# Kernel tuning notes

Hardware: AMD Instinct MI355X
Metric: run time of the kernel (lower is better)

## Reference

```python
import jax, jax.numpy as jnp
import numpy as np

N_NODES = 100000
N_EDGES = 1600000
IN_RAW = 64
HID = 128


def setup_inputs() -> dict:
    key = jax.random.key(0)
    ks = jax.random.split(key, 16)
    inp = {
        "x": jax.random.normal(ks[0], (N_NODES, IN_RAW), dtype=jnp.float32),
        "edge_index": jax.random.randint(ks[1], (2, N_EDGES), 0, N_NODES, dtype=jnp.int64),
        "user_ids": jax.random.randint(ks[2], (N_NODES,), 0, 10000, dtype=jnp.int64),
        "locations": jax.random.randint(ks[3], (N_NODES,), 0, 1000, dtype=jnp.int64),
        "time_features": jax.random.normal(ks[4], (N_NODES, 4), dtype=jnp.float32),
        # embeddings / encoders
        "user_emb_table": jax.random.normal(ks[5], (10000, 32), dtype=jnp.float32) * 0.02,
        "loc_emb_table": jax.random.normal(ks[6], (1000, 16), dtype=jnp.float32) * 0.02,
        "W_time": jax.random.normal(ks[7], (4, 16), dtype=jnp.float32) * 0.1,
        "b_time": jnp.zeros((16,), dtype=jnp.float32),
        # SAGEConv 1: lin_l (aggregated, with bias), lin_r (root, no bias)
        "W1_l": jax.random.normal(ks[8], (HID, HID), dtype=jnp.float32) * (1.0 / np.sqrt(HID)),
        "b1": jnp.zeros((HID,), dtype=jnp.float32),
        "W1_r": jax.random.normal(ks[9], (HID, HID), dtype=jnp.float32) * (1.0 / np.sqrt(HID)),
        # SAGEConv 2
        "W2_l": jax.random.normal(ks[10], (HID, HID), dtype=jnp.float32) * (1.0 / np.sqrt(HID)),
        "b2": jnp.zeros((HID,), dtype=jnp.float32),
        "W2_r": jax.random.normal(ks[11], (HID, HID), dtype=jnp.float32) * (1.0 / np.sqrt(HID)),
        # classifier
        "Wc": jax.random.normal(ks[12], (HID, 1), dtype=jnp.float32) * (1.0 / np.sqrt(HID)),
        "bc": jnp.zeros((1,), dtype=jnp.float32),
    }
    return inp


def _sage_conv(h, src, dst, W_l, b_l, W_r, n_nodes):
    # mean aggregation of source features onto targets (PyG SAGEConv default)
    msg_sum = jax.ops.segment_sum(h[src], dst, num_segments=n_nodes)  # [N, D]
    deg = jax.ops.segment_sum(jnp.ones((src.shape[0],), h.dtype), dst, num_segments=n_nodes)
    agg = msg_sum / jnp.maximum(deg, 1.0)[:, None]
    return agg @ W_l + b_l + h @ W_r


def reference(x, edge_index, user_ids, locations, time_features,
              user_emb_table, loc_emb_table, W_time, b_time,
              W1_l, b1, W1_r, W2_l, b2, W2_r, Wc, bc):
    n = x.shape[0]
    src, dst = edge_index[0], edge_index[1]
    user_emb = user_emb_table[user_ids]            # [N, 32]
    loc_emb = loc_emb_table[locations]             # [N, 16]
    time_emb = time_features @ W_time + b_time     # [N, 16]
    h = jnp.concatenate([x, user_emb, loc_emb, time_emb], axis=-1)  # [N, 128]
    h = jax.nn.relu(_sage_conv(h, src, dst, W1_l, b1, W1_r, n))  # dropout = identity (eval)
    h = jax.nn.relu(_sage_conv(h, src, dst, W2_l, b2, W2_r, n))
    return jax.nn.sigmoid(h @ Wc + bc)  # [N, 1]
```

## Files before the change

### kernel.cpp

```cpp
#include <hip/hip_runtime.h>
#include <math.h>

#define N_NODES 100000
#define HID 128
#define NB 782
#define CAP 4096
#define NBLK 256
#define BTILE 6250
#define SUBCAP 32
#define SCAP 3072
#define WPB 64

typedef __attribute__((ext_vector_type(8))) short bf16x8;
typedef __attribute__((ext_vector_type(4))) float f32x4;
typedef __attribute__((ext_vector_type(2))) float f32x2;

__device__ __forceinline__ unsigned short f2bf(float f) {
  union { float f; unsigned u; } v; v.f = f;
  unsigned r = v.u + 0x7FFFu + ((v.u >> 16) & 1u);
  return (unsigned short)(r >> 16);
}
__device__ __forceinline__ unsigned packbf(float lo, float hi) {
  return (unsigned)f2bf(lo) | ((unsigned)f2bf(hi) << 16);
}
__device__ __forceinline__ unsigned pkfp8x4(float a, float b, float c, float d) {
  int v = __builtin_amdgcn_cvt_pk_fp8_f32(a, b, 0, false);
  v = __builtin_amdgcn_cvt_pk_fp8_f32(c, d, v, true);
  return (unsigned)v;
}
__device__ __forceinline__ float bflo(unsigned u) {
  union { unsigned u; float f; } v; v.u = u << 16; return v.f;
}
__device__ __forceinline__ float bfhi(unsigned u) {
  union { unsigned u; float f; } v; v.u = u & 0xFFFF0000u; return v.f;
}
__device__ __forceinline__ void acc_add_fp8(float* a, unsigned w) {
  f32x2 p0 = __builtin_amdgcn_cvt_pk_f32_fp8((int)w, false);
  f32x2 p1 = __builtin_amdgcn_cvt_pk_f32_fp8((int)w, true);
  a[0] += p0.x; a[1] += p0.y; a[2] += p1.x; a[3] += p1.y;
}
__device__ __forceinline__ void acc_add_row(float* a, uint4 u) {
  acc_add_fp8(a + 0, u.x);
  acc_add_fp8(a + 4, u.y);
  acc_add_fp8(a + 8, u.z);
  acc_add_fp8(a + 12, u.w);
}

__global__ __launch_bounds__(256) void k_embed(
    const float* __restrict__ x, const int* __restrict__ uid,
    const int* __restrict__ lid, const float* __restrict__ timef,
    const float* __restrict__ utab, const float* __restrict__ ltab,
    const float* __restrict__ Wt, const float* __restrict__ bt,
    unsigned short* __restrict__ h0, unsigned char* __restrict__ h0f8) {
  int t = threadIdx.x;
  int v = blockIdx.x * 16 + (t >> 4);
  int g = t & 15;
  if (v >= N_NODES) return;
  float val[8];
  if (g < 8) {
    const float4* xp = (const float4*)&x[(size_t)v * 64 + g * 8];
    float4 a = xp[0], b = xp[1];
    val[0] = a.x; val[1] = a.y; val[2] = a.z; val[3] = a.w;
    val[4] = b.x; val[5] = b.y; val[6] = b.z; val[7] = b.w;
  } else if (g < 12) {
    const float4* up = (const float4*)&utab[(size_t)uid[v] * 32 + (g - 8) * 8];
    float4 a = up[0], b = up[1];
    val[0] = a.x; val[1] = a.y; val[2] = a.z; val[3] = a.w;
    val[4] = b.x; val[5] = b.y; val[6] = b.z; val[7] = b.w;
  } else if (g < 14) {
    const float4* lp = (const float4*)&ltab[(size_t)lid[v] * 16 + (g - 12) * 8];
    float4 a = lp[0], b = lp[1];
    val[0] = a.x; val[1] = a.y; val[2] = a.z; val[3] = a.w;
    val[4] = b.x; val[5] = b.y; val[6] = b.z; val[7] = b.w;
  } else {
    int c0 = (g - 14) * 8;
    float4 tf = *(const float4*)&timef[(size_t)v * 4];
#pragma unroll
    for (int i = 0; i < 8; ++i) {
      int c = c0 + i;
      val[i] = bt[c] + tf.x * Wt[c] + tf.y * Wt[16 + c] + tf.z * Wt[32 + c] +
               tf.w * Wt[48 + c];
    }
  }
  uint4 ob;
  ob.x = packbf(val[0], val[1]);
  ob.y = packbf(val[2], val[3]);
  ob.z = packbf(val[4], val[5]);
  ob.w = packbf(val[6], val[7]);
  *(uint4*)&h0[(size_t)v * 128 + g * 8] = ob;
  uint2 of;
  of.x = pkfp8x4(val[0], val[1], val[2], val[3]);
  of.y = pkfp8x4(val[4], val[5], val[6], val[7]);
  *(uint2*)&h0f8[(size_t)v * 128 + g * 8] = of;
}

__global__ __launch_bounds__(512) void k_bucket(
    const int* __restrict__ src, const int* __restrict__ dst,
    int* __restrict__ gcnt, unsigned* __restrict__ bdata2, int E) {
  __shared__ int hcnt[NB];
  int t = threadIdx.x;
  int blk = blockIdx.x;
  int e0 = blk * BTILE;
  int e1 = min(e0 + BTILE, E);
  for (int i = t; i < NB; i += 512) hcnt[i] = 0;
  __syncthreads();
#pragma unroll 4
  for (int e = e0 + t; e < e1; e += 512) {
    int d = dst[e], s = src[e];
    int b = d >> 7;
    int pos = atomicAdd(&hcnt[b], 1);
    if (pos < SUBCAP)
      bdata2[((size_t)blk * NB + b) * SUBCAP + pos] =
          ((unsigned)s << 7) | (unsigned)(d & 127);
  }
  __syncthreads();
  for (int i = t; i < NB; i += 512)
    gcnt[blk * NB + i] = hcnt[i];
}

__global__ __launch_bounds__(256) void k_bfill(
    const int* __restrict__ gcnt, const unsigned* __restrict__ bdata2,
    int* __restrict__ rstart, int* __restrict__ rdeg, int* __restrict__ col,
    const float* __restrict__ W1l, const float* __restrict__ W1r,
    const float* __restrict__ W2l, const float* __restrict__ W2r,
    unsigned short* __restrict__ WT) {
  int b = blockIdx.x;
  int t = threadIdx.x;
  if (b >= NB) {
    int lin = ((b - NB) * 256 + t) * 4;
    int m = lin >> 14;
    int rem = lin & 16383;
    int f = rem >> 7;
    int k0 = rem & 127;
    const float* W = (m == 0) ? W1l : (m == 1) ? W1r : (m == 2) ? W2l : W2r;
    unsigned short o[4];
#pragma unroll
    for (int j = 0; j < 4; ++j) o[j] = f2bf(W[(size_t)(k0 + j) * 128 + f]);
    uint2 pk;
    pk.x = (unsigned)o[0] | ((unsigned)o[1] << 16);
    pk.y = (unsigned)o[2] | ((unsigned)o[3] << 16);
    *(uint2*)&WT[m * 16384 + f * 128 + k0] = pk;
    return;
  }
  __shared__ unsigned sdata[SCAP];
  __shared__ int soff[NBLK];
  __shared__ int scnt[NBLK];
  __shared__ int wsum[4];
  __shared__ int lcnt[128];
  __shared__ int wtot;
  int lane = t & 63, wv = t >> 6;

  int c = (t < NBLK) ? min(gcnt[t * NB + b], SUBCAP) : 0;
  int x = c;
#pragma unroll
  for (int off = 1; off < 64; off <<= 1) {
    int v = __shfl_up(x, off);
    if (lane >= off) x += v;
  }
  if (lane == 63) wsum[wv] = x;
  __syncthreads();
  int add = 0;
#pragma unroll
  for (int k = 0; k < 4; ++k)
    if (k < wv) add += wsum[k];
  x += add;
  int tot = min(wsum[0] + wsum[1] + wsum[2] + wsum[3], SCAP);
  if (t < NBLK) { soff[t] = x - c; scnt[t] = c; }
  if (t < 128) lcnt[t] = 0;
  __syncthreads();

  for (int i = t; i < NBLK * 8; i += 256) {
    int j = i >> 3, p4 = (i & 7) * 4;
    int cj = scnt[j];
    if (p4 < cj) {
      uint4 v = *(const uint4*)&bdata2[((size_t)j * NB + b) * SUBCAP + p4];
      int bs = soff[j] + p4;
      int n = min(4, cj - p4);
      unsigned vv[4] = {v.x, v.y, v.z, v.w};
#pragma unroll
      for (int e = 0; e < 4; ++e)
        if (e < n && bs + e < SCAP) sdata[bs + e] = vv[e];
    }
  }
  __syncthreads();

  for (int i = t; i < tot; i += 256) atomicAdd(&lcnt[sdata[i] & 127u], 1);
  __syncthreads();

  int node0 = b * 128;
  int base = b * CAP;
  if (t < 128) {
    int cc = lcnt[t];
    int xx = cc;
#pragma unroll
    for (int off = 1; off < 64; off <<= 1) {
      int v = __shfl_up(xx, off);
      if (lane >= off) xx += v;
    }
    if (t == 63) wtot = xx;
    __syncthreads();
    if (t >= 64) xx += wtot;
    int excl = xx - cc;
    if (node0 + t < N_NODES) {
      rstart[node0 + t] = base + excl;
      rdeg[node0 + t] = cc;
    }
    lcnt[t] = excl;
  } else {
    __syncthreads();
  }
  __syncthreads();
  for (int i = t; i < tot; i += 256) {
    unsigned v = sdata[i];
    int pos = base + atomicAdd(&lcnt[v & 127u], 1);
    col[pos] = (int)(v >> 7);
  }
}

__global__ __launch_bounds__(256) void k_agg(
    const unsigned char* __restrict__ hf8, const int* __restrict__ rstart,
    const int* __restrict__ rdeg, const int* __restrict__ col,
    unsigned short* __restrict__ agg) {
  int t = threadIdx.x;
  int v = blockIdx.x * 32 + (t >> 3);
  int q = t & 7;
  if (v >= N_NODES) return;
  int s0 = rstart[v];
  int deg = rdeg[v];
  int s1 = s0 + deg;
  const uint4* h8 = (const uint4*)hf8;
  float acc[16];
#pragma unroll
  for (int i = 0; i < 16; ++i) acc[i] = 0.f;
  int j = s0;
  for (; j + 4 <= s1; j += 4) {
    uint4 r0 = h8[(size_t)col[j] * 8 + q];
    uint4 r1 = h8[(size_t)col[j + 1] * 8 + q];
    uint4 r2 = h8[(size_t)col[j + 2] * 8 + q];
    uint4 r3 = h8[(size_t)col[j + 3] * 8 + q];
    acc_add_row(acc, r0);
    acc_add_row(acc, r1);
    acc_add_row(acc, r2);
    acc_add_row(acc, r3);
  }
  for (; j < s1; ++j) acc_add_row(acc, h8[(size_t)col[j] * 8 + q]);
  float inv = 1.f / (float)(deg > 0 ? deg : 1);
  uint4 o0, o1;
  o0.x = packbf(acc[0] * inv, acc[1] * inv);
  o0.y = packbf(acc[2] * inv, acc[3] * inv);
  o0.z = packbf(acc[4] * inv, acc[5] * inv);
  o0.w = packbf(acc[6] * inv, acc[7] * inv);
  o1.x = packbf(acc[8] * inv, acc[9] * inv);
  o1.y = packbf(acc[10] * inv, acc[11] * inv);
  o1.z = packbf(acc[12] * inv, acc[13] * inv);
  o1.w = packbf(acc[14] * inv, acc[15] * inv);
  ((uint4*)agg)[(size_t)v * 16 + q * 2] = o0;
  ((uint4*)agg)[(size_t)v * 16 + q * 2 + 1] = o1;
}

template <bool CLS>
__global__ __launch_bounds__(256, 4) void k_gemm(
    const unsigned short* __restrict__ agg, const unsigned short* __restrict__ hin,
    const unsigned short* __restrict__ WlT, const unsigned short* __restrict__ WrT,
    const float* __restrict__ bias, unsigned short* __restrict__ hout,
    unsigned char* __restrict__ houtf8,
    const float* __restrict__ Wc, const float* __restrict__ bc,
    float* __restrict__ out) {
  __shared__ unsigned short SB[2 * 64 * 136];
  unsigned short* As = SB;
  unsigned short* Hs = SB + 64 * 136;
  unsigned short* Ot = SB;
  float* zred = (float*)SB;
  int t = threadIdx.x;
  int lane = t & 63;
  int wave = t >> 6;
  int wn = wave * 32;
  int l15 = lane & 15;
  int quad = lane >> 4;
  int mbase = blockIdx.x * 64;

  {
    int r = t >> 2, seg = t & 3;
    int gn = mbase + r;
    uint4 av[4], hv[4];
    if (gn < N_NODES) {
      const uint4* ap = (const uint4*)(agg + (size_t)gn * 128 + seg * 32);
      const uint4* hp = (const uint4*)(hin + (size_t)gn * 128 + seg * 32);
#pragma unroll
      for (int i = 0; i < 4; ++i) { av[i] = ap[i]; hv[i] = hp[i]; }
    } else {
#pragma unroll
      for (int i = 0; i < 4; ++i) { av[i] = make_uint4(0,0,0,0); hv[i] = make_uint4(0,0,0,0); }
    }
#pragma unroll
    for (int i = 0; i < 4; ++i) {
      *(uint4*)&As[r * 136 + seg * 32 + i * 8] = av[i];
      *(uint4*)&Hs[r * 136 + seg * 32 + i * 8] = hv[i];
    }
  }
  __syncthreads();

  f32x4 acc4[4][2];
#pragma unroll
  for (int i = 0; i < 4; ++i)
#pragma unroll
    for (int j = 0; j < 2; ++j) acc4[i][j] = (f32x4){0.f, 0.f, 0.f, 0.f};

#pragma unroll
  for (int ks = 0; ks < 4; ++ks) {
    int kb = ks * 32 + quad * 8;
    bf16x8 bL[2], bR[2];
#pragma unroll
    for (int jn = 0; jn < 2; ++jn) {
      int f = wn + jn * 16 + l15;
      bL[jn] = *(const bf16x8*)&WlT[(size_t)f * 128 + kb];
      bR[jn] = *(const bf16x8*)&WrT[(size_t)f * 128 + kb];
    }
    bf16x8 aA[4], aH[4];
#pragma unroll
    for (int im = 0; im < 4; ++im) {
      aA[im] = *(const bf16x8*)&As[(im * 16 + l15) * 136 + kb];
      aH[im] = *(const bf16x8*)&Hs[(im * 16 + l15) * 136 + kb];
    }
#pragma unroll
    for (int im = 0; im < 4; ++im)
#pragma unroll
      for (int jn = 0; jn < 2; ++jn)
        acc4[im][jn] = __builtin_amdgcn_mfma_f32_16x16x32_bf16(
            aA[im], bL[jn], acc4[im][jn], 0, 0, 0);
#pragma unroll
    for (int im = 0; im < 4; ++im)
#pragma unroll
      for (int jn = 0; jn < 2; ++jn)
        acc4[im][jn] = __builtin_amdgcn_mfma_f32_16x16x32_bf16(
            aH[im], bR[jn], acc4[im][jn], 0, 0, 0);
  }

  float bv[2];
#pragma unroll
  for (int jn = 0; jn < 2; ++jn) bv[jn] = bias[wn + jn * 16 + l15];

  __syncthreads();

  if (!CLS) {
#pragma unroll
    for (int im = 0; im < 4; ++im)
#pragma unroll
      for (int rr = 0; rr < 4; ++rr) {
        int rloc = im * 16 + quad * 4 + rr;
#pragma unroll
        for (int jn = 0; jn < 2; ++jn)
          Ot[rloc * 136 + wn + jn * 16 + l15] =
              f2bf(fmaxf(acc4[im][jn][rr] + bv[jn], 0.f));
      }
    __syncthreads();
    int r = t >> 2, seg = t & 3;
    int node = mbase + r;
    if (node < N_NODES) {
      uint4 d0[4];
      const uint4* srcp = (const uint4*)&Ot[r * 136 + seg * 32];
      uint4* dstp = (uint4*)&hout[(size_t)node * 128 + seg * 32];
#pragma unroll
      for (int i = 0; i < 4; ++i) { d0[i] = srcp[i]; dstp[i] = d0[i]; }
      unsigned w[8];
#pragma unroll
      for (int i = 0; i < 4; ++i) {
        unsigned u[4] = {d0[i].x, d0[i].y, d0[i].z, d0[i].w};
#pragma unroll
        for (int p = 0; p < 2; ++p) {
          w[i * 2 + p] = pkfp8x4(bflo(u[p * 2]), bfhi(u[p * 2]),
                                 bflo(u[p * 2 + 1]), bfhi(u[p * 2 + 1]));
        }
      }
      uint4* fp = (uint4*)&houtf8[(size_t)node * 128 + seg * 32];
      fp[0] = make_uint4(w[0], w[1], w[2], w[3]);
      fp[1] = make_uint4(w[4], w[5], w[6], w[7]);
    }
  } else {
    float wcv[2];
#pragma unroll
    for (int jn = 0; jn < 2; ++jn) wcv[jn] = Wc[wn + jn * 16 + l15];
#pragma unroll
    for (int im = 0; im < 4; ++im) {
#pragma unroll
      for (int rr = 0; rr < 4; ++rr) {
        float p = 0.f;
#pragma unroll
        for (int jn = 0; jn < 2; ++jn)
          p += fmaxf(acc4[im][jn][rr] + bv[jn], 0.f) * wcv[jn];
        p += __shfl_xor(p, 1);
        p += __shfl_xor(p, 2);
        p += __shfl_xor(p, 4);
        p += __shfl_xor(p, 8);
        if (l15 == 0) zred[wave * 64 + im * 16 + quad * 4 + rr] = p;
      }
    }
    __syncthreads();
    if (t < 64) {
      int node = mbase + t;
      if (node < N_NODES) {
        float z = zred[t] + zred[64 + t] + zred[128 + t] + zred[192 + t] + bc[0];
        out[node] = 1.f / (1.f + expf(-z));
      }
    }
  }
}

extern "C" void kernel_launch(void* const* d_in, const int* in_sizes, int n_in,
                              void* d_out, int out_size, void* d_ws, size_t ws_size,
                              hipStream_t stream) {
  const float* x     = (const float*)d_in[0];
  const int*   eidx  = (const int*)d_in[1];
  const int*   uid   = (const int*)d_in[2];
  const int*   lid   = (const int*)d_in[3];
  const float* timef = (const float*)d_in[4];
  const float* utab  = (const float*)d_in[5];
  const float* ltab  = (const float*)d_in[6];
  const float* Wt    = (const float*)d_in[7];
  const float* bt    = (const float*)d_in[8];
  const float* W1l   = (const float*)d_in[9];
  const float* b1    = (const float*)d_in[10];
  const float* W1r   = (const float*)d_in[11];
  const float* W2l   = (const float*)d_in[12];
  const float* b2    = (const float*)d_in[13];
  const float* W2r   = (const float*)d_in[14];
  const float* Wc    = (const float*)d_in[15];
  const float* bc    = (const float*)d_in[16];
  float* out = (float*)d_out;

  const int E = in_sizes[1] / 2;
  const int* src = eidx;
  const int* dst = eidx + E;

  char* ws = (char*)d_ws;
  size_t off = 0;
  auto alloc = [&](size_t bytes) -> void* {
    void* p = ws + off;
    off += (bytes + 255) & ~(size_t)255;
    return p;
  };
  const size_t HBYTES = (size_t)N_NODES * 128 * sizeof(unsigned short);
  const size_t FBYTES = (size_t)N_NODES * 128;
  unsigned short* h0  = (unsigned short*)alloc(HBYTES);
  unsigned short* h1  = (unsigned short*)alloc(HBYTES);
  unsigned short* agg = (unsigned short*)alloc(HBYTES);
  unsigned char* h0f8 = (unsigned char*)alloc(FBYTES);
  unsigned char* h1f8 = (unsigned char*)alloc(FBYTES);
  unsigned short* WT  = (unsigned short*)alloc(4 * 16384 * sizeof(unsigned short));
  unsigned* bdata2    = (unsigned*)alloc((size_t)NBLK * NB * SUBCAP * 4);
  int* gcnt           = (int*)alloc((size_t)NBLK * NB * 4);
  int* col            = (int*)alloc((size_t)NB * CAP * 4);
  int* rstart         = (int*)alloc((size_t)N_NODES * 4);
  int* rdeg           = (int*)alloc((size_t)N_NODES * 4);
  (void)ws_size; (void)n_in; (void)out_size;

  k_bucket<<<NBLK, 512, 0, stream>>>(src, dst, gcnt, bdata2, E);
  k_embed<<<(N_NODES + 15) / 16, 256, 0, stream>>>(x, uid, lid, timef, utab, ltab, Wt, bt,
                                                   h0, h0f8);
  k_bfill<<<NB + WPB, 256, 0, stream>>>(gcnt, bdata2, rstart, rdeg, col,
                                        W1l, W1r, W2l, W2r, WT);

  k_agg<<<(N_NODES + 31) / 32, 256, 0, stream>>>(h0f8, rstart, rdeg, col, agg);
  k_gemm<false><<<(N_NODES + 63) / 64, 256, 0, stream>>>(
      agg, h0, WT, WT + 16384, b1, h1, h1f8, nullptr, nullptr, nullptr);

  k_agg<<<(N_NODES + 31) / 32, 256, 0, stream>>>(h1f8, rstart, rdeg, col, agg);
  k_gemm<true><<<(N_NODES + 63) / 64, 256, 0, stream>>>(
      agg, h1, WT + 32768, WT + 49152, b2, nullptr, nullptr, Wc, bc, out);
}
```

Before: 284.9 us.

## Fuse neighbor aggregation into the SAGE GEMM and merge bucketing with embedding

The mean-aggregation gather now runs inside the GEMM kernel and writes the bf16 aggregate straight into shared memory, which removes the global agg buffer and its write-then-read round trip plus two kernel launches. Edge bucketing and node embedding are merged into one launch with a block-index split, and the embed path moves from 256 to 512 threads per block. The tradeoff is that the GEMM kernel now carries the irregular gather latency with only 256 threads per 64-row tile, which may hurt latency hiding compared with the separate aggregation kernel.

```diff
diff --git a/kernel.cpp b/kernel.cpp
--- a/kernel.cpp
+++ b/kernel.cpp
@@ -10,6 +10,7 @@
 #define SUBCAP 32
 #define SCAP 3072
 #define WPB 64
+#define EBLK 3125
 
 typedef __attribute__((ext_vector_type(8))) short bf16x8;
 typedef __attribute__((ext_vector_type(4))) float f32x4;
@@ -46,14 +47,37 @@
   acc_add_fp8(a + 12, u.w);
 }
 
-__global__ __launch_bounds__(256) void k_embed(
+__global__ __launch_bounds__(512) void k_bktembed(
+    const int* __restrict__ src, const int* __restrict__ dst,
+    int* __restrict__ gcnt, unsigned* __restrict__ bdata2, int E,
     const float* __restrict__ x, const int* __restrict__ uid,
     const int* __restrict__ lid, const float* __restrict__ timef,
     const float* __restrict__ utab, const float* __restrict__ ltab,
     const float* __restrict__ Wt, const float* __restrict__ bt,
     unsigned short* __restrict__ h0, unsigned char* __restrict__ h0f8) {
+  __shared__ int hcnt[NB];
   int t = threadIdx.x;
-  int v = blockIdx.x * 16 + (t >> 4);
+  if (blockIdx.x < NBLK) {
+    int blk = blockIdx.x;
+    int e0 = blk * BTILE;
+    int e1 = min(e0 + BTILE, E);
+    for (int i = t; i < NB; i += 512) hcnt[i] = 0;
+    __syncthreads();
+#pragma unroll 4
+    for (int e = e0 + t; e < e1; e += 512) {
+      int d = dst[e], s = src[e];
+      int b = d >> 7;
+      int pos = atomicAdd(&hcnt[b], 1);
+      if (pos < SUBCAP)
+        bdata2[((size_t)blk * NB + b) * SUBCAP + pos] =
+            ((unsigned)s << 7) | (unsigned)(d & 127);
+    }
+    __syncthreads();
+    for (int i = t; i < NB; i += 512)
+      gcnt[blk * NB + i] = hcnt[i];
+    return;
+  }
+  int v = (blockIdx.x - NBLK) * 32 + (t >> 4);
   int g = t & 15;
   if (v >= N_NODES) return;
   float val[8];
@@ -94,30 +118,6 @@
   *(uint2*)&h0f8[(size_t)v * 128 + g * 8] = of;
 }
 
-__global__ __launch_bounds__(512) void k_bucket(
-    const int* __restrict__ src, const int* __restrict__ dst,
-    int* __restrict__ gcnt, unsigned* __restrict__ bdata2, int E) {
-  __shared__ int hcnt[NB];
-  int t = threadIdx.x;
-  int blk = blockIdx.x;
-  int e0 = blk * BTILE;
-  int e1 = min(e0 + BTILE, E);
-  for (int i = t; i < NB; i += 512) hcnt[i] = 0;
-  __syncthreads();
-#pragma unroll 4
-  for (int e = e0 + t; e < e1; e += 512) {
-    int d = dst[e], s = src[e];
-    int b = d >> 7;
-    int pos = atomicAdd(&hcnt[b], 1);
-    if (pos < SUBCAP)
-      bdata2[((size_t)blk * NB + b) * SUBCAP + pos] =
-          ((unsigned)s << 7) | (unsigned)(d & 127);
-  }
-  __syncthreads();
-  for (int i = t; i < NB; i += 512)
-    gcnt[blk * NB + i] = hcnt[i];
-}
-
 __global__ __launch_bounds__(256) void k_bfill(
     const int* __restrict__ gcnt, const unsigned* __restrict__ bdata2,
     int* __restrict__ rstart, int* __restrict__ rdeg, int* __restrict__ col,
@@ -217,50 +217,11 @@
   }
 }
 
-__global__ __launch_bounds__(256) void k_agg(
+template <bool CLS>
+__global__ __launch_bounds__(256, 4) void k_aggemm(
     const unsigned char* __restrict__ hf8, const int* __restrict__ rstart,
     const int* __restrict__ rdeg, const int* __restrict__ col,
-    unsigned short* __restrict__ agg) {
-  int t = threadIdx.x;
-  int v = blockIdx.x * 32 + (t >> 3);
-  int q = t & 7;
-  if (v >= N_NODES) return;
-  int s0 = rstart[v];
-  int deg = rdeg[v];
-  int s1 = s0 + deg;
-  const uint4* h8 = (const uint4*)hf8;
-  float acc[16];
-#pragma unroll
-  for (int i = 0; i < 16; ++i) acc[i] = 0.f;
-  int j = s0;
-  for (; j + 4 <= s1; j += 4) {
-    uint4 r0 = h8[(size_t)col[j] * 8 + q];
-    uint4 r1 = h8[(size_t)col[j + 1] * 8 + q];
-    uint4 r2 = h8[(size_t)col[j + 2] * 8 + q];
-    uint4 r3 = h8[(size_t)col[j + 3] * 8 + q];
-    acc_add_row(acc, r0);
-    acc_add_row(acc, r1);
-    acc_add_row(acc, r2);
-    acc_add_row(acc, r3);
-  }
-  for (; j < s1; ++j) acc_add_row(acc, h8[(size_t)col[j] * 8 + q]);
-  float inv = 1.f / (float)(deg > 0 ? deg : 1);
-  uint4 o0, o1;
-  o0.x = packbf(acc[0] * inv, acc[1] * inv);
-  o0.y = packbf(acc[2] * inv, acc[3] * inv);
-  o0.z = packbf(acc[4] * inv, acc[5] * inv);
-  o0.w = packbf(acc[6] * inv, acc[7] * inv);
-  o1.x = packbf(acc[8] * inv, acc[9] * inv);
-  o1.y = packbf(acc[10] * inv, acc[11] * inv);
-  o1.z = packbf(acc[12] * inv, acc[13] * inv);
-  o1.w = packbf(acc[14] * inv, acc[15] * inv);
-  ((uint4*)agg)[(size_t)v * 16 + q * 2] = o0;
-  ((uint4*)agg)[(size_t)v * 16 + q * 2 + 1] = o1;
-}
-
-template <bool CLS>
-__global__ __launch_bounds__(256, 4) void k_gemm(
-    const unsigned short* __restrict__ agg, const unsigned short* __restrict__ hin,
+    const unsigned short* __restrict__ hin,
     const unsigned short* __restrict__ WlT, const unsigned short* __restrict__ WrT,
     const float* __restrict__ bias, unsigned short* __restrict__ hout,
     unsigned char* __restrict__ houtf8,
@@ -279,25 +240,64 @@
   int quad = lane >> 4;
   int mbase = blockIdx.x * 64;
 
+  int sr = t >> 2, sseg = t & 3;
+  uint4 hv[4];
   {
-    int r = t >> 2, seg = t & 3;
-    int gn = mbase + r;
-    uint4 av[4], hv[4];
+    int gn = mbase + sr;
     if (gn < N_NODES) {
-      const uint4* ap = (const uint4*)(agg + (size_t)gn * 128 + seg * 32);
-      const uint4* hp = (const uint4*)(hin + (size_t)gn * 128 + seg * 32);
-#pragma unroll
-      for (int i = 0; i < 4; ++i) { av[i] = ap[i]; hv[i] = hp[i]; }
+      const uint4* hp = (const uint4*)(hin + (size_t)gn * 128 + sseg * 32);
+#pragma unroll
+      for (int i = 0; i < 4; ++i) hv[i] = hp[i];
     } else {
 #pragma unroll
-      for (int i = 0; i < 4; ++i) { av[i] = make_uint4(0,0,0,0); hv[i] = make_uint4(0,0,0,0); }
-    }
-#pragma unroll
-    for (int i = 0; i < 4; ++i) {
-      *(uint4*)&As[r * 136 + seg * 32 + i * 8] = av[i];
-      *(uint4*)&Hs[r * 136 + seg * 32 + i * 8] = hv[i];
-    }
-  }
+      for (int i = 0; i < 4; ++i) hv[i] = make_uint4(0, 0, 0, 0);
+    }
+  }
+
+  const uint4* h8 = (const uint4*)hf8;
+#pragma unroll
+  for (int half = 0; half < 2; ++half) {
+    int r = half * 32 + (t >> 3);
+    int q = t & 7;
+    int v = mbase + r;
+    float acc[16];
+#pragma unroll
+    for (int i = 0; i < 16; ++i) acc[i] = 0.f;
+    float inv = 0.f;
+    if (v < N_NODES) {
+      int s0 = rstart[v];
+      int deg = rdeg[v];
+      int s1 = s0 + deg;
+      int j = s0;
+      for (; j + 4 <= s1; j += 4) {
+        uint4 r0 = h8[(size_t)col[j] * 8 + q];
+        uint4 r1 = h8[(size_t)col[j + 1] * 8 + q];
+        uint4 r2 = h8[(size_t)col[j + 2] * 8 + q];
+        uint4 r3 = h8[(size_t)col[j + 3] * 8 + q];
+        acc_add_row(acc, r0);
+        acc_add_row(acc, r1);
+        acc_add_row(acc, r2);
+        acc_add_row(acc, r3);
+      }
+      for (; j < s1; ++j) acc_add_row(acc, h8[(size_t)col[j] * 8 + q]);
+      inv = 1.f / (float)(deg > 0 ? deg : 1);
+    }
+    uint4 o0, o1;
+    o0.x = packbf(acc[0] * inv, acc[1] * inv);
+    o0.y = packbf(acc[2] * inv, acc[3] * inv);
+    o0.z = packbf(acc[4] * inv, acc[5] * inv);
+    o0.w = packbf(acc[6] * inv, acc[7] * inv);
+    o1.x = packbf(acc[8] * inv, acc[9] * inv);
+    o1.y = packbf(acc[10] * inv, acc[11] * inv);
+    o1.z = packbf(acc[12] * inv, acc[13] * inv);
+    o1.w = packbf(acc[14] * inv, acc[15] * inv);
+    *(uint4*)&As[r * 136 + q * 16] = o0;
+    *(uint4*)&As[r * 136 + q * 16 + 8] = o1;
+  }
+
+#pragma unroll
+  for (int i = 0; i < 4; ++i)
+    *(uint4*)&Hs[sr * 136 + sseg * 32 + i * 8] = hv[i];
   __syncthreads();
 
   f32x4 acc4[4][2];
@@ -443,7 +443,6 @@
   const size_t FBYTES = (size_t)N_NODES * 128;
   unsigned short* h0  = (unsigned short*)alloc(HBYTES);
   unsigned short* h1  = (unsigned short*)alloc(HBYTES);
-  unsigned short* agg = (unsigned short*)alloc(HBYTES);
   unsigned char* h0f8 = (unsigned char*)alloc(FBYTES);
   unsigned char* h1f8 = (unsigned char*)alloc(FBYTES);
   unsigned short* WT  = (unsigned short*)alloc(4 * 16384 * sizeof(unsigned short));
@@ -454,17 +453,17 @@
   int* rdeg           = (int*)alloc((size_t)N_NODES * 4);
   (void)ws_size; (void)n_in; (void)out_size;
 
-  k_bucket<<<NBLK, 512, 0, stream>>>(src, dst, gcnt, bdata2, E);
-  k_embed<<<(N_NODES + 15) / 16, 256, 0, stream>>>(x, uid, lid, timef, utab, ltab, Wt, bt,
-                                                   h0, h0f8);
+  k_bktembed<<<NBLK + EBLK, 512, 0, stream>>>(src, dst, gcnt, bdata2, E,
+                                              x, uid, lid, timef, utab, ltab,
+                                              Wt, bt, h0, h0f8);
   k_bfill<<<NB + WPB, 256, 0, stream>>>(gcnt, bdata2, rstart, rdeg, col,
                                         W1l, W1r, W2l, W2r, WT);
 
-  k_agg<<<(N_NODES + 31) / 32, 256, 0, stream>>>(h0f8, rstart, rdeg, col, agg);
-  k_gemm<false><<<(N_NODES + 63) / 64, 256, 0, stream>>>(
-      agg, h0, WT, WT + 16384, b1, h1, h1f8, nullptr, nullptr, nullptr);
-
-  k_agg<<<(N_NODES + 31) / 32, 256, 0, stream>>>(h1f8, rstart, rdeg, col, agg);
-  k_gemm<true><<<(N_NODES + 63) / 64, 256, 0, stream>>>(
-      agg, h1, WT + 32768, WT + 49152, b2, nullptr, nullptr, Wc, bc, out);
-}
+  k_aggemm<false><<<(N_NODES + 63) / 64, 256, 0, stream>>>(
+      h0f8, rstart, rdeg, col, h0, WT, WT + 16384, b1, h1, h1f8,
+      nullptr, nullptr, nullptr);
+
+  k_aggemm<true><<<(N_NODES + 63) / 64, 256, 0, stream>>>(
+      h1f8, rstart, rdeg, col, h1, WT + 32768, WT + 49152, b2,
+      nullptr, nullptr, Wc, bc, out);
+}
```

Result: faster. 268.3 us (-5.8%).
